# Kernel tuning notes

Measured on AMD Instinct MI355X. Metric: run time of the kernel, lower is better.

The kernel has to match this reference:

```python
import jax, jax.numpy as jnp
import numpy as np

B, T, D, H, K = 8, 4096, 768, 12, 64
EPS_WKV = 1e-9
EPS_GN = 1e-5


def setup_inputs() -> dict:
    key = jax.random.key(0)
    ks = jax.random.split(key, 12)
    x = jax.random.normal(ks[0], (B, T, D), jnp.float32)
    # linear projection weights (torch nn.Linear stores [out, in]; y = x @ W.T)
    W_r = jax.random.normal(ks[1], (D, D), jnp.float32) * 0.02
    W_k = jax.random.normal(ks[2], (D, D), jnp.float32) * 0.02
    W_v = jax.random.normal(ks[3], (D, D), jnp.float32) * 0.02
    W_o = jax.random.normal(ks[4], (D, D), jnp.float32) * 0.02
    time_mix_r = jax.random.uniform(ks[5], (D,), jnp.float32)
    time_mix_k = jax.random.uniform(ks[6], (D,), jnp.float32)
    time_mix_v = jax.random.uniform(ks[7], (D,), jnp.float32)
    # around the module's init values (time_decay ~ -0.075, time_first ~ 0.15 at layer 6/12)
    time_decay = -0.075 + 0.1 * jax.random.normal(ks[8], (H, K), jnp.float32)
    time_first = 0.15 + 0.1 * jax.random.normal(ks[9], (H, K), jnp.float32)
    gn_weight = jnp.ones((D,), jnp.float32)
    gn_bias = jnp.zeros((D,), jnp.float32)
    return {
        "x": x,
        "time_mix_r": time_mix_r, "time_mix_k": time_mix_k, "time_mix_v": time_mix_v,
        "time_decay": time_decay, "time_first": time_first,
        "W_r": W_r, "W_k": W_k, "W_v": W_v, "W_o": W_o,
        "gn_weight": gn_weight, "gn_bias": gn_bias,
    }


def reference(x, time_mix_r, time_mix_k, time_mix_v, time_decay, time_first,
              W_r, W_k, W_v, W_o, gn_weight, gn_bias):
    Bx, Tx, Dx = x.shape
    Hx, Kx = time_decay.shape
    # token-shift: previous timestep (zero-initialized state)
    x_prev = jnp.concatenate([jnp.zeros_like(x[:, :1]), x[:, :-1]], axis=1)
    xr = x * time_mix_r + x_prev * (1.0 - time_mix_r)
    xk = x * time_mix_k + x_prev * (1.0 - time_mix_k)
    xv = x * time_mix_v + x_prev * (1.0 - time_mix_v)
    r = jax.nn.sigmoid(xr @ W_r.T).reshape(Bx, Tx, Hx, Kx)
    k = (xk @ W_k.T).reshape(Bx, Tx, Hx, Kx)
    v = (xv @ W_v.T).reshape(Bx, Tx, Hx, Kx)

    w = jnp.exp(-jnp.exp(time_decay))   # [H,K] decay per channel
    eu = jnp.exp(time_first)            # [H,K] bonus for current token

    def step(carry, kv_t):
        num, den = carry                # each [B,H,K]
        k_t, v_t = kv_t                 # each [B,H,K]
        ek = jnp.exp(k_t)
        wkv = (num + eu * ek * v_t) / (den + eu * ek + EPS_WKV)
        return (num * w + ek * v_t, den * w + ek), wkv

    k_tm = jnp.moveaxis(k, 1, 0)        # [T,B,H,K]
    v_tm = jnp.moveaxis(v, 1, 0)
    init = (jnp.zeros((Bx, Hx, Kx), x.dtype), jnp.zeros((Bx, Hx, Kx), x.dtype))
    _, wkv = jax.lax.scan(step, init, (k_tm, v_tm))
    out = jnp.moveaxis(wkv, 0, 1)       # [B,T,H,K]

    y = r * out                         # [B,T,H,K]
    # torch GroupNorm(H, D) on [B, D, T]: normalize each group over (K channels x T steps)
    mean = y.mean(axis=(1, 3), keepdims=True)
    var = y.var(axis=(1, 3), keepdims=True)
    y = (y - mean) * jax.lax.rsqrt(var + EPS_GN)
    y = y * gn_weight.reshape(1, 1, Hx, Kx) + gn_bias.reshape(1, 1, Hx, Kx)
    return y.reshape(Bx, Tx, Dx) @ W_o.T
```

## Files before the change

kernel.cpp:

```cpp
#include <hip/hip_runtime.h>
#include <hip/hip_bf16.h>
#include <cstdint>

#define B_ 8
#define T_ 4096
#define D_ 768
#define H_ 12
#define M_ (B_*T_)
#define CHUNKS 64
#define CLEN 64
#define WELEM (D_*D_)
#define NCH (B_*H_*64)

typedef __attribute__((ext_vector_type(8))) short bf16x8;
typedef __attribute__((ext_vector_type(4))) float f32x4;

static __device__ __forceinline__ unsigned short f2bf(float f) {
  __hip_bfloat16 h = __float2bfloat16(f);
  return __builtin_bit_cast(unsigned short, h);
}
static __device__ __forceinline__ float bf2f(unsigned short u) {
  unsigned v = ((unsigned)u) << 16;
  return __builtin_bit_cast(float, v);
}

static __device__ __forceinline__ void async16(const void* g, void* l) {
  __builtin_amdgcn_global_load_lds(
      (const __attribute__((address_space(1))) unsigned int*)g,
      (__attribute__((address_space(3))) unsigned int*)l, 16, 0, 0);
}

__global__ __launch_bounds__(256) void zero_out_kernel(float* __restrict__ out, size_t n4) {
  size_t gid = (size_t)blockIdx.x * 256 + threadIdx.x;
  if (gid < n4) *(float4*)(out + gid * 4) = make_float4(0.f, 0.f, 0.f, 0.f);
}

__global__ __launch_bounds__(256) void mix_kernel(
    const float* __restrict__ x, const float* __restrict__ tmr,
    const float* __restrict__ tmk, const float* __restrict__ tmv,
    unsigned short* __restrict__ xr, unsigned short* __restrict__ xk,
    unsigned short* __restrict__ xv) {
  size_t gid = (size_t)blockIdx.x * 256 + threadIdx.x;
  size_t idx4 = gid * 4;
  int d = (int)(idx4 % D_);
  size_t row = idx4 / D_;
  int t = (int)(row & (T_ - 1));
  float4 xc = *(const float4*)(x + idx4);
  float4 xp = make_float4(0.f, 0.f, 0.f, 0.f);
  if (t > 0) xp = *(const float4*)(x + idx4 - D_);
  float4 mr = *(const float4*)(tmr + d);
  float4 mk = *(const float4*)(tmk + d);
  float4 mv = *(const float4*)(tmv + d);
  ushort4 orr, okk, ovv;
  orr.x = f2bf(xc.x*mr.x + xp.x*(1.f-mr.x));
  orr.y = f2bf(xc.y*mr.y + xp.y*(1.f-mr.y));
  orr.z = f2bf(xc.z*mr.z + xp.z*(1.f-mr.z));
  orr.w = f2bf(xc.w*mr.w + xp.w*(1.f-mr.w));
  okk.x = f2bf(xc.x*mk.x + xp.x*(1.f-mk.x));
  okk.y = f2bf(xc.y*mk.y + xp.y*(1.f-mk.y));
  okk.z = f2bf(xc.z*mk.z + xp.z*(1.f-mk.z));
  okk.w = f2bf(xc.w*mk.w + xp.w*(1.f-mk.w));
  ovv.x = f2bf(xc.x*mv.x + xp.x*(1.f-mv.x));
  ovv.y = f2bf(xc.y*mv.y + xp.y*(1.f-mv.y));
  ovv.z = f2bf(xc.z*mv.z + xp.z*(1.f-mv.z));
  ovv.w = f2bf(xc.w*mv.w + xp.w*(1.f-mv.w));
  *(ushort4*)(xr + idx4) = orr;
  *(ushort4*)(xk + idx4) = okk;
  *(ushort4*)(xv + idx4) = ovv;
}

__global__ __launch_bounds__(256) void wconv_kernel(
    const float* __restrict__ a, const float* __restrict__ b,
    const float* __restrict__ c, const float* __restrict__ d,
    unsigned short* __restrict__ o) {
  size_t gid = (size_t)blockIdx.x * 256 + threadIdx.x;
  size_t idx4 = gid * 4;
  size_t mi = idx4 / WELEM;
  size_t off = idx4 % WELEM;
  const float* src = (mi == 0) ? a : (mi == 1) ? b : (mi == 2) ? c : d;
  float4 v = *(const float4*)(src + off);
  ushort4 u;
  u.x = f2bf(v.x); u.y = f2bf(v.y); u.z = f2bf(v.z); u.w = f2bf(v.w);
  *(ushort4*)(o + idx4) = u;
}

template<int ACT, int OBF>
__global__ __launch_bounds__(256) void gemm_nt(
    const unsigned short* __restrict__ A,
    const unsigned short* __restrict__ Bw,
    void* __restrict__ Cv, int M, int N, int Kd) {
  __shared__ __align__(16) unsigned short As[128 * 32];
  __shared__ __align__(16) unsigned short Bs[128 * 32];
  const int tid = threadIdx.x;
  const int wave = tid >> 6, lane = tid & 63;
  const int quad = lane >> 4, l16 = lane & 15;
  const int m0 = blockIdx.y * 128, n0 = blockIdx.x * 128;
  const int wm = (wave & 1) * 64, wn = (wave >> 1) * 64;

  f32x4 acc[4][4] = {};

  for (int kb = 0; kb < Kd; kb += 32) {
    __syncthreads();
#pragma unroll
    for (int j = 0; j < 2; ++j) {
      int chunk = wave * 128 + j * 64 + lane;
      int row = chunk >> 2, kc = chunk & 3;
      const unsigned short* ga = A  + ((size_t)(m0 + row) * Kd + kb + kc * 8);
      async16(ga, &As[chunk * 8]);
      const unsigned short* gb = Bw + ((size_t)(n0 + row) * Kd + kb + kc * 8);
      async16(gb, &Bs[chunk * 8]);
    }
    __syncthreads();

    bf16x8 a[4], b[4];
#pragma unroll
    for (int i = 0; i < 4; ++i)
      a[i] = *(const bf16x8*)&As[(wm + i * 16 + l16) * 32 + quad * 8];
#pragma unroll
    for (int i = 0; i < 4; ++i)
      b[i] = *(const bf16x8*)&Bs[(wn + i * 16 + l16) * 32 + quad * 8];
#pragma unroll
    for (int i = 0; i < 4; ++i)
#pragma unroll
      for (int j = 0; j < 4; ++j)
        acc[i][j] = __builtin_amdgcn_mfma_f32_16x16x32_bf16(a[i], b[j], acc[i][j], 0, 0, 0);
  }

#pragma unroll
  for (int i = 0; i < 4; ++i) {
    int rowb = m0 + wm + i * 16 + quad * 4;
#pragma unroll
    for (int j = 0; j < 4; ++j) {
      int col = n0 + wn + j * 16 + l16;
#pragma unroll
      for (int r = 0; r < 4; ++r) {
        float v = acc[i][j][r];
        if (ACT == 1) v = 1.f / (1.f + __expf(-v));
        size_t idx = (size_t)(rowb + r) * N + col;
        if (OBF) ((unsigned short*)Cv)[idx] = f2bf(v);
        else     ((float*)Cv)[idx] = v;
      }
    }
  }
}

__global__ __launch_bounds__(256) void wkv_pass1(
    const unsigned short* __restrict__ Kb, const unsigned short* __restrict__ Vb,
    const float* __restrict__ td,
    float* __restrict__ sumN, float* __restrict__ sumD) {
  int gid = blockIdx.x * 256 + threadIdx.x;
  int k = gid & 63;
  int h = (gid >> 6) % H_;
  int tmp = (gid >> 6) / H_;
  int b = tmp % B_;
  int c = tmp / B_;
  float w = __expf(-__expf(td[h * 64 + k]));
  size_t base = ((size_t)(b * T_ + c * CLEN)) * D_ + h * 64 + k;
  float num = 0.f, den = 0.f;
#pragma unroll 8
  for (int i = 0; i < CLEN; ++i) {
    float kk = bf2f(Kb[base + (size_t)i * D_]);
    float vv = bf2f(Vb[base + (size_t)i * D_]);
    float ek = __expf(kk);
    num = num * w + ek * vv;
    den = den * w + ek;
  }
  sumN[gid] = num;
  sumD[gid] = den;
}

__global__ __launch_bounds__(256) void wkv_pass2(
    const float* __restrict__ sumN, const float* __restrict__ sumD,
    const float* __restrict__ td,
    float* __restrict__ prefN, float* __restrict__ prefD,
    float* __restrict__ gstats) {
  int tid = blockIdx.x * 256 + threadIdx.x;
  if (blockIdx.x == 0 && threadIdx.x < 192) gstats[threadIdx.x] = 0.f;
  int k = tid & 63;
  int h = (tid >> 6) % H_;
  float w = __expf(-__expf(td[h * 64 + k]));
  float wL = w;
#pragma unroll
  for (int i = 0; i < 6; ++i) wL *= wL;
  float n = 0.f, d = 0.f;
  for (int c = 0; c < CHUNKS; ++c) {
    int j = c * NCH + tid;
    prefN[j] = n; prefD[j] = d;
    n = n * wL + sumN[j];
    d = d * wL + sumD[j];
  }
}

__global__ __launch_bounds__(256) void wkv_pass3(
    const unsigned short* __restrict__ Kb, const unsigned short* __restrict__ Vb,
    unsigned short* __restrict__ RY,
    const float* __restrict__ td, const float* __restrict__ tf,
    const float* __restrict__ prefN, const float* __restrict__ prefD,
    float* __restrict__ gsum, float* __restrict__ gsq) {
  int gid = blockIdx.x * 256 + threadIdx.x;
  int k = gid & 63;
  int h = (gid >> 6) % H_;
  int tmp = (gid >> 6) / H_;
  int b = tmp % B_;
  int c = tmp / B_;
  float w = __expf(-__expf(td[h * 64 + k]));
  float eu = __expf(tf[h * 64 + k]);
  float num = prefN[gid], den = prefD[gid];
  size_t base = ((size_t)(b * T_ + c * CLEN)) * D_ + h * 64 + k;
  float s1 = 0.f, s2 = 0.f;
#pragma unroll 4
  for (int i = 0; i < CLEN; ++i) {
    size_t idx = base + (size_t)i * D_;
    float kk = bf2f(Kb[idx]);
    float vv = bf2f(Vb[idx]);
    float rr = bf2f(RY[idx]);
    float ek = __expf(kk);
    float wkv = (num + eu * ek * vv) / (den + eu * ek + 1e-9f);
    unsigned short ybf = f2bf(rr * wkv);
    RY[idx] = ybf;
    float y = bf2f(ybf);
    s1 += y; s2 += y * y;
    num = num * w + ek * vv;
    den = den * w + ek;
  }
#pragma unroll
  for (int off = 32; off; off >>= 1) {
    s1 += __shfl_down(s1, off);
    s2 += __shfl_down(s2, off);
  }
  if (k == 0) {
    atomicAdd(&gsum[b * H_ + h], s1);
    atomicAdd(&gsq [b * H_ + h], s2);
  }
}

__global__ __launch_bounds__(256) void gn_kernel(
    const unsigned short* __restrict__ Y, const float* __restrict__ gsum,
    const float* __restrict__ gsq, const float* __restrict__ gw,
    const float* __restrict__ gb, unsigned short* __restrict__ Ybf) {
  size_t gid = (size_t)blockIdx.x * 256 + threadIdx.x;
  size_t idx4 = gid * 4;
  int d = (int)(idx4 % D_);
  size_t row = idx4 / D_;
  int b = (int)(row >> 12);
  int h = d >> 6;
  int g = b * H_ + h;
  const float inv = 1.f / (float)(T_ * 64);
  float mean = gsum[g] * inv;
  float var = gsq[g] * inv - mean * mean;
  float rstd = rsqrtf(var + 1e-5f);
  ushort4 yu = *(const ushort4*)(Y + idx4);
  float4 wv = *(const float4*)(gw + d);
  float4 bv = *(const float4*)(gb + d);
  ushort4 o;
  o.x = f2bf((bf2f(yu.x) - mean) * rstd * wv.x + bv.x);
  o.y = f2bf((bf2f(yu.y) - mean) * rstd * wv.y + bv.y);
  o.z = f2bf((bf2f(yu.z) - mean) * rstd * wv.z + bv.z);
  o.w = f2bf((bf2f(yu.w) - mean) * rstd * wv.w + bv.w);
  *(ushort4*)(Ybf + idx4) = o;
}

extern "C" void kernel_launch(void* const* d_in, const int* in_sizes, int n_in,
                              void* d_out, int out_size, void* d_ws, size_t ws_size,
                              hipStream_t stream) {
  (void)in_sizes; (void)n_in;
  const float* x   = (const float*)d_in[0];
  const float* tmr = (const float*)d_in[1];
  const float* tmk = (const float*)d_in[2];
  const float* tmv = (const float*)d_in[3];
  const float* td  = (const float*)d_in[4];
  const float* tf  = (const float*)d_in[5];
  const float* Wr  = (const float*)d_in[6];
  const float* Wk  = (const float*)d_in[7];
  const float* Wv  = (const float*)d_in[8];
  const float* Wo  = (const float*)d_in[9];
  const float* gw  = (const float*)d_in[10];
  const float* gb  = (const float*)d_in[11];
  float* out = (float*)d_out;

  constexpr size_t MD = (size_t)M_ * D_;
  constexpr size_t NEED = 4 * (MD * 2)
                        + (size_t)4 * WELEM * 2
                        + 4 * ((size_t)CHUNKS * NCH * 4)
                        + 1024;
  if (ws_size < NEED) {
    zero_out_kernel<<<(int)((MD / 4 + 255) / 256), 256, 0, stream>>>(out, MD / 4);
    return;
  }

  char* ws = (char*)d_ws;
  unsigned short* XR = (unsigned short*)ws; ws += MD * 2;
  unsigned short* XK = (unsigned short*)ws; ws += MD * 2;
  unsigned short* XV = (unsigned short*)ws; ws += MD * 2;
  unsigned short* Rb = (unsigned short*)ws; ws += MD * 2;
  unsigned short* Wb = (unsigned short*)ws; ws += (size_t)4 * WELEM * 2;
  float* sumN  = (float*)ws; ws += (size_t)CHUNKS * NCH * 4;
  float* sumD  = (float*)ws; ws += (size_t)CHUNKS * NCH * 4;
  float* prefN = (float*)ws; ws += (size_t)CHUNKS * NCH * 4;
  float* prefD = (float*)ws; ws += (size_t)CHUNKS * NCH * 4;
  float* gstats = (float*)ws; ws += 1024;
  unsigned short* Kb = XR;
  unsigned short* Vb = XK;
  unsigned short* Yb = XV;

  mix_kernel<<<(int)(MD / 1024), 256, 0, stream>>>(x, tmr, tmk, tmv, XR, XK, XV);
  wconv_kernel<<<(4 * WELEM / 4) / 256, 256, 0, stream>>>(Wr, Wk, Wv, Wo, Wb);

  dim3 ggrid(D_ / 128, M_ / 128);
  gemm_nt<1, 1><<<ggrid, 256, 0, stream>>>(XR, Wb,             Rb, M_, D_, D_);
  gemm_nt<0, 1><<<ggrid, 256, 0, stream>>>(XK, Wb + WELEM,     Kb, M_, D_, D_);
  gemm_nt<0, 1><<<ggrid, 256, 0, stream>>>(XV, Wb + 2 * WELEM, Vb, M_, D_, D_);

  wkv_pass1<<<(CHUNKS * NCH) / 256, 256, 0, stream>>>(Kb, Vb, td, sumN, sumD);
  wkv_pass2<<<NCH / 256, 256, 0, stream>>>(sumN, sumD, td, prefN, prefD, gstats);
  wkv_pass3<<<(CHUNKS * NCH) / 256, 256, 0, stream>>>(Kb, Vb, Rb, td, tf,
                                                      prefN, prefD, gstats, gstats + 96);
  gn_kernel<<<(int)(MD / 1024), 256, 0, stream>>>(Rb, gstats, gstats + 96, gw, gb, Yb);

  gemm_nt<0, 0><<<ggrid, 256, 0, stream>>>(Yb, Wb + 3 * WELEM, out, M_, D_, D_);
}
```

Before: 578.9 us.

## Retile GEMM with swizzled LDS, XCD remap, staged stores; vectorize WKV scan passes

```diff
diff --git a/kernel.cpp b/kernel.cpp
--- a/kernel.cpp
+++ b/kernel.cpp
@@ -7,8 +7,8 @@
 #define D_ 768
 #define H_ 12
 #define M_ (B_*T_)
-#define CHUNKS 64
-#define CLEN 64
+#define CHUNKS 256
+#define CLEN 16
 #define WELEM (D_*D_)
 #define NCH (B_*H_*64)
 
@@ -89,56 +89,93 @@
     const unsigned short* __restrict__ A,
     const unsigned short* __restrict__ Bw,
     void* __restrict__ Cv, int M, int N, int Kd) {
-  __shared__ __align__(16) unsigned short As[128 * 32];
-  __shared__ __align__(16) unsigned short Bs[128 * 32];
+  __shared__ __align__(16) unsigned short smem[128 * 128];
+  unsigned short* As = smem;
+  unsigned short* Bs = smem + 128 * 64;
   const int tid = threadIdx.x;
   const int wave = tid >> 6, lane = tid & 63;
   const int quad = lane >> 4, l16 = lane & 15;
-  const int m0 = blockIdx.y * 128, n0 = blockIdx.x * 128;
+
+  int nwg = gridDim.x * gridDim.y;
+  int lin = blockIdx.y * gridDim.x + blockIdx.x;
+  int q = nwg >> 3, r = nwg & 7;
+  int xcd = lin & 7, off = lin >> 3;
+  int swz = (xcd < r ? xcd * (q + 1) : r * (q + 1) + (xcd - r) * q) + off;
+  const int m0 = (swz / gridDim.x) * 128;
+  const int n0 = (swz % gridDim.x) * 128;
   const int wm = (wave & 1) * 64, wn = (wave >> 1) * 64;
 
   f32x4 acc[4][4] = {};
 
-  for (int kb = 0; kb < Kd; kb += 32) {
+  for (int kb = 0; kb < Kd; kb += 64) {
     __syncthreads();
 #pragma unroll
-    for (int j = 0; j < 2; ++j) {
-      int chunk = wave * 128 + j * 64 + lane;
-      int row = chunk >> 2, kc = chunk & 3;
-      const unsigned short* ga = A  + ((size_t)(m0 + row) * Kd + kb + kc * 8);
-      async16(ga, &As[chunk * 8]);
-      const unsigned short* gb = Bw + ((size_t)(n0 + row) * Kd + kb + kc * 8);
-      async16(gb, &Bs[chunk * 8]);
+    for (int j = 0; j < 4; ++j) {
+      int chunk = j * 256 + tid;
+      int row = chunk >> 3, slot = chunk & 7;
+      int ks = slot ^ (row & 7);
+      async16(A  + ((size_t)(m0 + row) * Kd + kb + ks * 8), &As[chunk * 8]);
+      async16(Bw + ((size_t)(n0 + row) * Kd + kb + ks * 8), &Bs[chunk * 8]);
     }
     __syncthreads();
 
-    bf16x8 a[4], b[4];
-#pragma unroll
-    for (int i = 0; i < 4; ++i)
-      a[i] = *(const bf16x8*)&As[(wm + i * 16 + l16) * 32 + quad * 8];
-#pragma unroll
-    for (int i = 0; i < 4; ++i)
-      b[i] = *(const bf16x8*)&Bs[(wn + i * 16 + l16) * 32 + quad * 8];
-#pragma unroll
-    for (int i = 0; i < 4; ++i)
-#pragma unroll
-      for (int j = 0; j < 4; ++j)
-        acc[i][j] = __builtin_amdgcn_mfma_f32_16x16x32_bf16(a[i], b[j], acc[i][j], 0, 0, 0);
-  }
-
-#pragma unroll
-  for (int i = 0; i < 4; ++i) {
-    int rowb = m0 + wm + i * 16 + quad * 4;
-#pragma unroll
-    for (int j = 0; j < 4; ++j) {
-      int col = n0 + wn + j * 16 + l16;
-#pragma unroll
-      for (int r = 0; r < 4; ++r) {
-        float v = acc[i][j][r];
-        if (ACT == 1) v = 1.f / (1.f + __expf(-v));
-        size_t idx = (size_t)(rowb + r) * N + col;
-        if (OBF) ((unsigned short*)Cv)[idx] = f2bf(v);
-        else     ((float*)Cv)[idx] = v;
+#pragma unroll
+    for (int kk = 0; kk < 2; ++kk) {
+      bf16x8 a[4], b[4];
+#pragma unroll
+      for (int i = 0; i < 4; ++i) {
+        int ra = wm + i * 16 + l16;
+        a[i] = *(const bf16x8*)&As[ra * 64 + (((kk * 4 + quad) ^ (ra & 7)) * 8)];
+        int rb = wn + i * 16 + l16;
+        b[i] = *(const bf16x8*)&Bs[rb * 64 + (((kk * 4 + quad) ^ (rb & 7)) * 8)];
+      }
+#pragma unroll
+      for (int i = 0; i < 4; ++i)
+#pragma unroll
+        for (int jj = 0; jj < 4; ++jj)
+          acc[i][jj] = __builtin_amdgcn_mfma_f32_16x16x32_bf16(a[i], b[jj], acc[i][jj], 0, 0, 0);
+    }
+  }
+
+  if (OBF) {
+    __syncthreads();
+    unsigned short* Cs = smem;
+#pragma unroll
+    for (int i = 0; i < 4; ++i) {
+#pragma unroll
+      for (int jj = 0; jj < 4; ++jj) {
+        int col = wn + jj * 16 + l16;
+#pragma unroll
+        for (int rr = 0; rr < 4; ++rr) {
+          int row = wm + i * 16 + quad * 4 + rr;
+          float v = acc[i][jj][rr];
+          if (ACT == 1) v = 1.f / (1.f + __expf(-v));
+          int cg = (col >> 3) ^ (row & 7);
+          Cs[row * 128 + cg * 8 + (col & 7)] = f2bf(v);
+        }
+      }
+    }
+    __syncthreads();
+#pragma unroll
+    for (int g = 0; g < 8; ++g) {
+      int gi = g * 256 + tid;
+      int row = gi >> 4, cg = gi & 15;
+      int sg = cg ^ (row & 7);
+      bf16x8 vv = *(const bf16x8*)&Cs[row * 128 + sg * 8];
+      *(bf16x8*)((unsigned short*)Cv + (size_t)(m0 + row) * N + n0 + cg * 8) = vv;
+    }
+  } else {
+#pragma unroll
+    for (int i = 0; i < 4; ++i) {
+      int rowb = m0 + wm + i * 16 + quad * 4;
+#pragma unroll
+      for (int jj = 0; jj < 4; ++jj) {
+        int col = n0 + wn + jj * 16 + l16;
+#pragma unroll
+        for (int rr = 0; rr < 4; ++rr) {
+          float v = acc[i][jj][rr];
+          ((float*)Cv)[(size_t)(rowb + rr) * N + col] = v;
+        }
       }
     }
   }
@@ -149,24 +186,36 @@
     const float* __restrict__ td,
     float* __restrict__ sumN, float* __restrict__ sumD) {
   int gid = blockIdx.x * 256 + threadIdx.x;
-  int k = gid & 63;
-  int h = (gid >> 6) % H_;
-  int tmp = (gid >> 6) / H_;
+  int kg = gid & 7;
+  int tmp = gid >> 3;
+  int h = tmp % H_;
+  tmp /= H_;
   int b = tmp % B_;
   int c = tmp / B_;
-  float w = __expf(-__expf(td[h * 64 + k]));
-  size_t base = ((size_t)(b * T_ + c * CLEN)) * D_ + h * 64 + k;
-  float num = 0.f, den = 0.f;
-#pragma unroll 8
+  const float* tdp = td + h * 64 + kg * 8;
+  float w[8], num[8], den[8];
+#pragma unroll
+  for (int j = 0; j < 8; ++j) {
+    w[j] = __expf(-__expf(tdp[j]));
+    num[j] = 0.f; den[j] = 0.f;
+  }
+  size_t base = ((size_t)(b * T_ + c * CLEN)) * D_ + h * 64 + kg * 8;
+#pragma unroll 4
   for (int i = 0; i < CLEN; ++i) {
-    float kk = bf2f(Kb[base + (size_t)i * D_]);
-    float vv = bf2f(Vb[base + (size_t)i * D_]);
-    float ek = __expf(kk);
-    num = num * w + ek * vv;
-    den = den * w + ek;
-  }
-  sumN[gid] = num;
-  sumD[gid] = den;
+    bf16x8 k8 = *(const bf16x8*)(Kb + base + (size_t)i * D_);
+    bf16x8 v8 = *(const bf16x8*)(Vb + base + (size_t)i * D_);
+#pragma unroll
+    for (int j = 0; j < 8; ++j) {
+      float ek = __expf(bf2f((unsigned short)k8[j]));
+      num[j] = num[j] * w[j] + ek * bf2f((unsigned short)v8[j]);
+      den[j] = den[j] * w[j] + ek;
+    }
+  }
+  int ob = ((c * B_ + b) * H_ + h) * 64 + kg * 8;
+  *(float4*)(sumN + ob)     = make_float4(num[0], num[1], num[2], num[3]);
+  *(float4*)(sumN + ob + 4) = make_float4(num[4], num[5], num[6], num[7]);
+  *(float4*)(sumD + ob)     = make_float4(den[0], den[1], den[2], den[3]);
+  *(float4*)(sumD + ob + 4) = make_float4(den[4], den[5], den[6], den[7]);
 }
 
 __global__ __launch_bounds__(256) void wkv_pass2(
@@ -181,7 +230,7 @@
   float w = __expf(-__expf(td[h * 64 + k]));
   float wL = w;
 #pragma unroll
-  for (int i = 0; i < 6; ++i) wL *= wL;
+  for (int i = 0; i < 4; ++i) wL *= wL;
   float n = 0.f, d = 0.f;
   for (int c = 0; c < CHUNKS; ++c) {
     int j = c * NCH + tid;
@@ -198,37 +247,58 @@
     const float* __restrict__ prefN, const float* __restrict__ prefD,
     float* __restrict__ gsum, float* __restrict__ gsq) {
   int gid = blockIdx.x * 256 + threadIdx.x;
-  int k = gid & 63;
-  int h = (gid >> 6) % H_;
-  int tmp = (gid >> 6) / H_;
+  int kg = gid & 7;
+  int tmp = gid >> 3;
+  int h = tmp % H_;
+  tmp /= H_;
   int b = tmp % B_;
   int c = tmp / B_;
-  float w = __expf(-__expf(td[h * 64 + k]));
-  float eu = __expf(tf[h * 64 + k]);
-  float num = prefN[gid], den = prefD[gid];
-  size_t base = ((size_t)(b * T_ + c * CLEN)) * D_ + h * 64 + k;
+  const float* tdp = td + h * 64 + kg * 8;
+  const float* tfp = tf + h * 64 + kg * 8;
+  float w[8], eu[8], num[8], den[8];
+  int sb = ((c * B_ + b) * H_ + h) * 64 + kg * 8;
+  float4 n0 = *(const float4*)(prefN + sb), n1 = *(const float4*)(prefN + sb + 4);
+  float4 d0 = *(const float4*)(prefD + sb), d1 = *(const float4*)(prefD + sb + 4);
+  num[0]=n0.x; num[1]=n0.y; num[2]=n0.z; num[3]=n0.w;
+  num[4]=n1.x; num[5]=n1.y; num[6]=n1.z; num[7]=n1.w;
+  den[0]=d0.x; den[1]=d0.y; den[2]=d0.z; den[3]=d0.w;
+  den[4]=d1.x; den[5]=d1.y; den[6]=d1.z; den[7]=d1.w;
+#pragma unroll
+  for (int j = 0; j < 8; ++j) {
+    w[j]  = __expf(-__expf(tdp[j]));
+    eu[j] = __expf(tfp[j]);
+  }
+  size_t base = ((size_t)(b * T_ + c * CLEN)) * D_ + h * 64 + kg * 8;
   float s1 = 0.f, s2 = 0.f;
 #pragma unroll 4
   for (int i = 0; i < CLEN; ++i) {
     size_t idx = base + (size_t)i * D_;
-    float kk = bf2f(Kb[idx]);
-    float vv = bf2f(Vb[idx]);
-    float rr = bf2f(RY[idx]);
-    float ek = __expf(kk);
-    float wkv = (num + eu * ek * vv) / (den + eu * ek + 1e-9f);
-    unsigned short ybf = f2bf(rr * wkv);
-    RY[idx] = ybf;
-    float y = bf2f(ybf);
-    s1 += y; s2 += y * y;
-    num = num * w + ek * vv;
-    den = den * w + ek;
-  }
-#pragma unroll
-  for (int off = 32; off; off >>= 1) {
-    s1 += __shfl_down(s1, off);
-    s2 += __shfl_down(s2, off);
-  }
-  if (k == 0) {
+    bf16x8 k8 = *(const bf16x8*)(Kb + idx);
+    bf16x8 v8 = *(const bf16x8*)(Vb + idx);
+    bf16x8 r8 = *(const bf16x8*)(RY + idx);
+    bf16x8 y8;
+#pragma unroll
+    for (int j = 0; j < 8; ++j) {
+      float kk = bf2f((unsigned short)k8[j]);
+      float vv = bf2f((unsigned short)v8[j]);
+      float rr = bf2f((unsigned short)r8[j]);
+      float ek = __expf(kk);
+      float wkv = (num[j] + eu[j] * ek * vv) / (den[j] + eu[j] * ek + 1e-9f);
+      unsigned short ybf = f2bf(rr * wkv);
+      y8[j] = (short)ybf;
+      float y = bf2f(ybf);
+      s1 += y; s2 += y * y;
+      num[j] = num[j] * w[j] + ek * vv;
+      den[j] = den[j] * w[j] + ek;
+    }
+    *(bf16x8*)(RY + idx) = y8;
+  }
+#pragma unroll
+  for (int off = 4; off; off >>= 1) {
+    s1 += __shfl_xor(s1, off);
+    s2 += __shfl_xor(s2, off);
+  }
+  if (kg == 0) {
     atomicAdd(&gsum[b * H_ + h], s1);
     atomicAdd(&gsq [b * H_ + h], s2);
   }
@@ -311,10 +381,10 @@
   gemm_nt<0, 1><<<ggrid, 256, 0, stream>>>(XK, Wb + WELEM,     Kb, M_, D_, D_);
   gemm_nt<0, 1><<<ggrid, 256, 0, stream>>>(XV, Wb + 2 * WELEM, Vb, M_, D_, D_);
 
-  wkv_pass1<<<(CHUNKS * NCH) / 256, 256, 0, stream>>>(Kb, Vb, td, sumN, sumD);
+  wkv_pass1<<<(CHUNKS * NCH / 8) / 256, 256, 0, stream>>>(Kb, Vb, td, sumN, sumD);
   wkv_pass2<<<NCH / 256, 256, 0, stream>>>(sumN, sumD, td, prefN, prefD, gstats);
-  wkv_pass3<<<(CHUNKS * NCH) / 256, 256, 0, stream>>>(Kb, Vb, Rb, td, tf,
-                                                      prefN, prefD, gstats, gstats + 96);
+  wkv_pass3<<<(CHUNKS * NCH / 8) / 256, 256, 0, stream>>>(Kb, Vb, Rb, td, tf,
+                                                          prefN, prefD, gstats, gstats + 96);
   gn_kernel<<<(int)(MD / 1024), 256, 0, stream>>>(Rb, gstats, gstats + 96, gw, gb, Yb);
 
   gemm_nt<0, 0><<<ggrid, 256, 0, stream>>>(Yb, Wb + 3 * WELEM, out, M_, D_, D_);
```

New measurement: 538.3 us. 7.0% less time.
